# Performance work log

Hardware: AMD Instinct MI355X
Metric: run time of the kernel (lower is better)

Reference implementation:

```python
import jax, jax.numpy as jnp
import numpy as np

B, T, D, H = 512, 128, 128, 256  # batch, time_steps, features, hidden; T == D keeps the source's transpose/step quirk shape-consistent


def _lin_init(k, out_f, in_f):
    s = 1.0 / np.sqrt(in_f)
    k1, k2 = jax.random.split(k)
    w = jax.random.uniform(k1, (out_f, in_f), minval=-s, maxval=s, dtype=jnp.float32)
    b = jax.random.uniform(k2, (out_f,), minval=-s, maxval=s, dtype=jnp.float32)
    return w, b


def setup_inputs() -> dict:
    key = jax.random.key(0)
    ks = jax.random.split(key, 12)
    mask = (jax.random.uniform(ks[0], (B, T, D)) > 0.3).astype(jnp.float32)
    meas = jax.random.normal(ks[1], (B, T, D), dtype=jnp.float32)
    delta = jax.random.uniform(ks[2], (B, T, D), dtype=jnp.float32) * 5.0
    # interleave Mask/Measurement/Delta along dim 1: X[:, 0::3] == mask, etc.
    X = jnp.stack([mask, meas, delta], axis=2).reshape(B, 3 * T, D)
    X_mean = jax.random.normal(ks[3], (1, D, T), dtype=jnp.float32) * 0.1
    din = 2 * T + H  # cat(x, h, mask) per-step input size
    Wz, bz = _lin_init(ks[4], H, din)
    Wr, br = _lin_init(ks[5], H, din)
    Wh, bh = _lin_init(ks[6], H, din)
    Wgx, bgx = _lin_init(ks[7], T, T)   # FilterLinear (identity filter)
    Wgh, bgh = _lin_init(ks[8], H, T)
    Wfc, bfc = _lin_init(ks[9], 1, H)
    gamma_bn = jnp.ones((H,), jnp.float32)
    beta_bn = jnp.zeros((H,), jnp.float32)
    return dict(X=X, X_mean=X_mean, Wz=Wz, bz=bz, Wr=Wr, br=br, Wh=Wh, bh=bh,
                Wgx=Wgx, bgx=bgx, Wgh=Wgh, bgh=bgh,
                gamma_bn=gamma_bn, beta_bn=beta_bn, Wfc=Wfc, bfc=bfc)


def _grud_forward(X, X_mean, Wz, bz, Wr, br, Wh, bh, Wgx, bgx, Wgh, bgh,
                  gamma_bn, beta_bn, Wfc, bfc):
    Bs = X.shape[0]
    Mask = jnp.swapaxes(X[:, 0::3, :], 1, 2)  # (B, D, T) -- source scans over dim 1 after transpose
    Meas = jnp.swapaxes(X[:, 1::3, :], 1, 2)
    Delt = jnp.swapaxes(X[:, 2::3, :], 1, 2)
    # FilterLinear: weight elementwise-masked by identity
    Wgx_eff = jnp.eye(Wgx.shape[0], dtype=Wgx.dtype) * Wgx
    xs = (jnp.moveaxis(Meas, 1, 0),   # (steps, B, T); x_last_obsv == Measurement in the source
          jnp.moveaxis(Mask, 1, 0),
          jnp.moveaxis(Delt, 1, 0),
          X_mean[0])                  # (steps, T)
    h0 = jnp.zeros((Bs, Wgh.shape[0]), dtype=X.dtype)

    def step(h, inp):
        x, m, d, xm = inp
        dx = jnp.exp(-jax.nn.relu(d @ Wgx_eff.T + bgx))   # input decay
        dh = jnp.exp(-jax.nn.relu(d @ Wgh.T + bgh))       # hidden decay
        x = m * x + (1 - m) * (dx * x + (1 - dx) * xm[None, :])  # masked imputation (x_last_obsv == x)
        h = dh * h
        c = jnp.concatenate([x, h, m], axis=1)
        z = jax.nn.sigmoid(c @ Wz.T + bz)
        r = jax.nn.sigmoid(c @ Wr.T + br)
        ht = jnp.tanh(jnp.concatenate([x, r * h, m], axis=1) @ Wh.T + bh)
        h = (1 - z) * h + z * ht
        return h, None

    hT, _ = jax.lax.scan(step, h0, xs)
    # dropout = identity (eval); BatchNorm1d with batch statistics (train-mode math, biased var)
    mu = hT.mean(axis=0)
    var = ((hT - mu) ** 2).mean(axis=0)
    hn = (hT - mu) / jnp.sqrt(var + 1e-5) * gamma_bn + beta_bn
    return hn @ Wfc.T + bfc  # (B, 1)


def reference(X, X_mean, Wz, bz, Wr, br, Wh, bh, Wgx, bgx, Wgh, bgh,
              gamma_bn, beta_bn, Wfc, bfc):
    return _grud_forward(X, X_mean, Wz, bz, Wr, br, Wh, bh, Wgx, bgx,
                         Wgh, bgh, gamma_bn, beta_bn, Wfc, bfc)
```

## Files before the change

kernel.cpp:

```cpp
#include <hip/hip_runtime.h>
#include <stdint.h>


#define NSTEP 128
#define NBAT  512

typedef __attribute__((ext_vector_type(8))) short bf16x8;
typedef __attribute__((ext_vector_type(4))) float f32x4;

__device__ __forceinline__ float bf2f(unsigned short u) {
  union { unsigned int i; float f; } v; v.i = ((unsigned int)u) << 16; return v.f;
}
__device__ __forceinline__ unsigned short f2bf(float f) {
  union { float f; unsigned int i; } v; v.f = f;
  unsigned int x = v.i;
  return (unsigned short)((x + 0x7fffu + ((x >> 16) & 1u)) >> 16);
}
__device__ __forceinline__ unsigned int cvt_pk_bf16(float lo, float hi) {
  unsigned int r;
  asm("v_cvt_pk_bf16_f32 %0, %1, %2" : "=v"(r) : "v"(lo), "v"(hi));
  return r;
}
__device__ __forceinline__ float sigm(float x) { return 1.f / (1.f + __expf(-x)); }
__device__ __forceinline__ unsigned short us4_get(ushort4 v, int r) {
  return r == 0 ? v.x : r == 1 ? v.y : r == 2 ? v.z : v.w;
}
#define PINV(x) asm volatile("" : "+v"(x))
#define BSYNC() do { asm volatile("s_waitcnt lgkmcnt(0)" ::: "memory"); \
                     __builtin_amdgcn_s_barrier(); } while (0)

#define L2E  1.44269504088896f
#define L2E2 2.88539008177793f

__global__ void pack_w(const float* __restrict__ Wz, const float* __restrict__ Wr,
                       const float* __restrict__ Wh, const float* __restrict__ Wgh,
                       const float* __restrict__ bz, const float* __restrict__ br,
                       const float* __restrict__ bh, const float* __restrict__ bgh,
                       const float* __restrict__ Xmean,
                       unsigned short* __restrict__ Wpre, unsigned short* __restrict__ Wzrh,
                       unsigned short* __restrict__ WhhP, float* __restrict__ Bpre,
                       float* __restrict__ XmT) {
  int id = blockIdx.x * 256 + threadIdx.x;
  if (id < 1024 * 384) {
    int j = id / 384, k = id % 384;
    float v = 0.f;
    if (j < 768) {
      const float* W = (j < 256) ? Wz : (j < 512) ? Wr : Wh;
      int jj = j & 255;
      if (k < 128)      v = W[jj * 512 + k];
      else if (k < 256) v = W[jj * 512 + 384 + (k - 128)];
      v *= (j < 512) ? L2E : L2E2;
    } else {
      int jj = j - 768;
      if (k >= 256) v = Wgh[jj * 128 + (k - 256)];
    }
    Wpre[id] = f2bf(v);
    return;
  }
  int id2 = id - 1024 * 384;
  if (id2 < 512 * 256) {
    int j = id2 >> 8, i = id2 & 255;
    float v = (j < 256) ? Wz[j * 512 + 128 + i] : Wr[(j - 256) * 512 + 128 + i];
    Wzrh[id2] = f2bf(v * L2E);
    return;
  }
  int id3 = id2 - 512 * 256;
  if (id3 < 256 * 256) {
    int j = id3 >> 8, i = id3 & 255;
    WhhP[id3] = f2bf(Wh[j * 512 + 128 + i] * L2E2);
    return;
  }
  int id4 = id3 - 256 * 256;
  if (id4 < 1024) {
    float v = (id4 < 256) ? bz[id4] * L2E : (id4 < 512) ? br[id4 - 256] * L2E
            : (id4 < 768) ? bh[id4 - 512] * L2E2 : bgh[id4 - 768];
    Bpre[id4] = v;
    return;
  }
  int id5 = id4 - 1024;
  if (id5 < 128 * 128) {
    int t = id5 >> 7, s = id5 & 127;
    XmT[t * 128 + s] = Xmean[s * 128 + t];
  }
}

__global__ __launch_bounds__(128) void prep(const float* __restrict__ X,
                                            const float* __restrict__ XmT,
                                            const float* __restrict__ Wgx,
                                            const float* __restrict__ bgx,
                                            unsigned short* __restrict__ Cin) {
  __shared__ unsigned short lx[64][132], lm[64][132], ldl[64][132];
  int b = blockIdx.x >> 1, tc = blockIdx.x & 1;
  int s = threadIdx.x;
  const float* Xb = X + (size_t)b * 384 * 128;
  for (int tt = 0; tt < 64; ++tt) {
    int t = tc * 64 + tt;
    float m = Xb[(3 * t + 0) * 128 + s];
    float x = Xb[(3 * t + 1) * 128 + s];
    float d = Xb[(3 * t + 2) * 128 + s];
    float wg = Wgx[t * 128 + t];
    float bg = bgx[t];
    float dx = __expf(-fmaxf(d * wg + bg, 0.f));
    float xm = XmT[t * 128 + s];
    float xt = m * x + (1.f - m) * (dx * x + (1.f - dx) * xm);
    lx[tt][s]  = f2bf(xt);
    lm[tt][s]  = f2bf(m);
    ldl[tt][s] = f2bf(d);
  }
  __syncthreads();
  for (int s0 = 0; s0 < 128; s0 += 2) {
    int ss = s0 + (threadIdx.x >> 6);
    int t  = threadIdx.x & 63;
    size_t base = ((size_t)ss * NBAT + b) * 384;
    Cin[base +       tc * 64 + t] = lx[t][ss];
    Cin[base + 128 + tc * 64 + t] = lm[t][ss];
    Cin[base + 256 + tc * 64 + t] = ldl[t][ss];
  }
}

__global__ __launch_bounds__(256) void u_gemm(const unsigned short* __restrict__ Cin,
                                              const unsigned short* __restrict__ Wpre,
                                              const float* __restrict__ Bpre,
                                              unsigned short* __restrict__ Upre) {
  __shared__ unsigned short Ash[64][392];
  int s  = blockIdx.x >> 3;
  int bc = blockIdx.x & 7;
  int b0 = bc * 64;
  {
    int r = threadIdx.x >> 2, part = threadIdx.x & 3;
    const uint4* src = (const uint4*)(Cin + ((size_t)s * NBAT + b0 + r) * 384);
    uint4* dst = (uint4*)&Ash[r][0];
#pragma unroll
    for (int q = 0; q < 12; ++q) dst[part + q * 4] = src[part + q * 4];
  }
  __syncthreads();
  int wid = threadIdx.x >> 6, lane = threadIdx.x & 63;
  int col = lane & 15, kq = lane >> 4;

  if (wid < 3) {
    int jbase = wid * 256;
    bf16x8 af[4][8];
#pragma unroll
    for (int mt = 0; mt < 4; ++mt)
#pragma unroll
      for (int kt = 0; kt < 8; ++kt)
        af[mt][kt] = *(const bf16x8*)&Ash[mt * 16 + col][kt * 32 + kq * 8];
    for (int jt = 0; jt < 16; ++jt) {
      int j0 = jbase + jt * 16;
      const unsigned short* wrow = Wpre + (size_t)(j0 + col) * 384 + kq * 8;
      f32x4 C[4] = {{0,0,0,0},{0,0,0,0},{0,0,0,0},{0,0,0,0}};
#pragma unroll
      for (int kt = 0; kt < 8; ++kt) {
        bf16x8 bw = *(const bf16x8*)(wrow + kt * 32);
        C[0] = __builtin_amdgcn_mfma_f32_16x16x32_bf16(bw, af[0][kt], C[0], 0, 0, 0);
        C[1] = __builtin_amdgcn_mfma_f32_16x16x32_bf16(bw, af[1][kt], C[1], 0, 0, 0);
        C[2] = __builtin_amdgcn_mfma_f32_16x16x32_bf16(bw, af[2][kt], C[2], 0, 0, 0);
        C[3] = __builtin_amdgcn_mfma_f32_16x16x32_bf16(bw, af[3][kt], C[3], 0, 0, 0);
      }
      int jv = j0 + kq * 4;
      float4 bias = *(const float4*)&Bpre[jv];
#pragma unroll
      for (int mt = 0; mt < 4; ++mt) {
        int bt = bc * 4 + mt;
        ushort4 o;
        o.x = f2bf(C[mt][0] + bias.x); o.y = f2bf(C[mt][1] + bias.y);
        o.z = f2bf(C[mt][2] + bias.z); o.w = f2bf(C[mt][3] + bias.w);
        *(ushort4*)(Upre + (((size_t)s * 32 + bt) * 16 + col) * 1024 + jv) = o;
      }
    }
  } else {
    bf16x8 af[4][4];
#pragma unroll
    for (int mt = 0; mt < 4; ++mt)
#pragma unroll
      for (int kt = 0; kt < 4; ++kt)
        af[mt][kt] = *(const bf16x8*)&Ash[mt * 16 + col][256 + kt * 32 + kq * 8];
    for (int jt = 0; jt < 16; ++jt) {
      int j0 = 768 + jt * 16;
      const unsigned short* wrow = Wpre + (size_t)(j0 + col) * 384 + 256 + kq * 8;
      f32x4 C[4] = {{0,0,0,0},{0,0,0,0},{0,0,0,0},{0,0,0,0}};
#pragma unroll
      for (int kt = 0; kt < 4; ++kt) {
        bf16x8 bw = *(const bf16x8*)(wrow + kt * 32);
        C[0] = __builtin_amdgcn_mfma_f32_16x16x32_bf16(bw, af[0][kt], C[0], 0, 0, 0);
        C[1] = __builtin_amdgcn_mfma_f32_16x16x32_bf16(bw, af[1][kt], C[1], 0, 0, 0);
        C[2] = __builtin_amdgcn_mfma_f32_16x16x32_bf16(bw, af[2][kt], C[2], 0, 0, 0);
        C[3] = __builtin_amdgcn_mfma_f32_16x16x32_bf16(bw, af[3][kt], C[3], 0, 0, 0);
      }
      int jv = j0 + kq * 4;
      float4 bias = *(const float4*)&Bpre[jv];
#pragma unroll
      for (int mt = 0; mt < 4; ++mt) {
        int bt = bc * 4 + mt;
        ushort4 o;
        o.x = f2bf(__expf(-fmaxf(C[mt][0] + bias.x, 0.f)));
        o.y = f2bf(__expf(-fmaxf(C[mt][1] + bias.y, 0.f)));
        o.z = f2bf(__expf(-fmaxf(C[mt][2] + bias.z, 0.f)));
        o.w = f2bf(__expf(-fmaxf(C[mt][3] + bias.w, 0.f)));
        *(ushort4*)(Upre + (((size_t)s * 32 + bt) * 16 + col) * 1024 + jv) = o;
      }
    }
  }
}

__global__ __launch_bounds__(512, 2) void recur(const unsigned short* __restrict__ Upre,
                                                const unsigned short* __restrict__ Wzrh,
                                                const unsigned short* __restrict__ WhhP,
                                                float* __restrict__ hT) {
  __shared__ unsigned short hb[16 * 256];
  __shared__ unsigned short qb[16 * 256];
  __shared__ unsigned short WhL[65536];
  int bt = blockIdx.x, tid = threadIdx.x;
  int wid = tid >> 6, lane = tid & 63, col = lane & 15, kq = lane >> 4;
  const int hsw = (col & 7) << 4;

#pragma unroll
  for (int i = 0; i < 16; ++i) {
    int f = tid + i * 512;
    int row = f >> 5, c = f & 31;
    bf16x8 v = *(const bf16x8*)(WhhP + (size_t)f * 8);
    *(bf16x8*)((char*)WhL + row * 512 + ((c * 16) ^ ((row & 7) << 4))) = v;
  }
  for (int i = tid; i < 16 * 256; i += 512) hb[i] = 0;

  bf16x8 wzf[2][8], wrf[2][8];
#pragma unroll
  for (int mt = 0; mt < 2; ++mt)
#pragma unroll
    for (int kt = 0; kt < 8; ++kt) {
      int j = wid * 32 + mt * 16 + col;
      wzf[mt][kt] = *(const bf16x8*)(Wzrh + (size_t)j * 256 + kt * 32 + kq * 8);
      wrf[mt][kt] = *(const bf16x8*)(Wzrh + (size_t)(256 + j) * 256 + kt * 32 + kq * 8);
      PINV(wzf[mt][kt]);
      PINV(wrf[mt][kt]);
    }

  const int joff0 = wid * 32 + kq * 4;
  const int hs_lo = hsw & 48, hs_hi = hsw & 64;
  const int cq  = (kq * 16) ^ hs_lo;
  const int rbA = col * 512 + cq + hs_hi;
  const int rbB = col * 512 + cq - hs_hi;
  const int row0 = wid * 32 + col;
  const int wrbA = row0 * 512 + cq + hs_hi;
  const int wrbB = row0 * 512 + cq - hs_hi;
  const int wby0 = col * 512 + ((joff0 * 2) ^ hsw);
  const int wby1 = col * 512 + (((joff0 + 16) * 2) ^ hsw);

  const unsigned short* Ub0 = Upre + ((size_t)bt * 16 + col) * 1024;
  const size_t SS = 32 * 16 * 1024;

  ushort4 uz[2], ur[2], uh[2], ug[2];
#pragma unroll
  for (int mt = 0; mt < 2; ++mt) {
    uz[mt] = *(const ushort4*)(Ub0 + 0   + joff0 + mt * 16);
    ur[mt] = *(const ushort4*)(Ub0 + 256 + joff0 + mt * 16);
    uh[mt] = *(const ushort4*)(Ub0 + 512 + joff0 + mt * 16);
    ug[mt] = *(const ushort4*)(Ub0 + SS + 768 + joff0 + mt * 16);
  }
  const unsigned short* pnext = Ub0 + SS + joff0;
  const unsigned short* pg    = Ub0 + 2 * SS + 768 + joff0;
  f32x4 Hst[2] = {{0,0,0,0},{0,0,0,0}};
  float zk[2][4];
  BSYNC();

  for (int s = 0; s < NSTEP; ++s) {
    f32x4 Cz[2] = {{0,0,0,0},{0,0,0,0}}, Cr[2] = {{0,0,0,0},{0,0,0,0}};
#pragma unroll
    for (int kt = 0; kt < 8; ++kt) {
      bf16x8 b = *(const bf16x8*)((const char*)hb + ((kt & 1) ? rbB : rbA) + kt * 64);
      Cz[0] = __builtin_amdgcn_mfma_f32_16x16x32_bf16(wzf[0][kt], b, Cz[0], 0, 0, 0);
      Cr[0] = __builtin_amdgcn_mfma_f32_16x16x32_bf16(wrf[0][kt], b, Cr[0], 0, 0, 0);
      Cz[1] = __builtin_amdgcn_mfma_f32_16x16x32_bf16(wzf[1][kt], b, Cz[1], 0, 0, 0);
      Cr[1] = __builtin_amdgcn_mfma_f32_16x16x32_bf16(wrf[1][kt], b, Cr[1], 0, 0, 0);
    }
#pragma unroll
    for (int mt = 0; mt < 2; ++mt) {
      float qv[4];
#pragma unroll
      for (int r = 0; r < 4; ++r) {
        float xz = Cz[mt][r] + bf2f(us4_get(uz[mt], r));
        float xr = Cr[mt][r] + bf2f(us4_get(ur[mt], r));
        float zv = __builtin_amdgcn_rcpf(1.f + __builtin_amdgcn_exp2f(-xz));
        float rv = __builtin_amdgcn_rcpf(1.f + __builtin_amdgcn_exp2f(-xr));
        zk[mt][r] = zv;
        qv[r] = rv * Hst[mt][r];
      }
      uint2 qw;
      qw.x = cvt_pk_bf16(qv[0], qv[1]);
      qw.y = cvt_pk_bf16(qv[2], qv[3]);
      *(uint2*)((char*)qb + (mt ? wby1 : wby0)) = qw;
    }
#pragma unroll
    for (int mt = 0; mt < 2; ++mt) {
      uz[mt] = *(const ushort4*)(pnext + 0   + mt * 16);
      ur[mt] = *(const ushort4*)(pnext + 256 + mt * 16);
    }
    BSYNC();
    f32x4 Ch[2] = {{0,0,0,0},{0,0,0,0}};
#pragma unroll
    for (int kt = 0; kt < 8; ++kt) {
      int ro = ((kt & 1) ? rbB : rbA) + kt * 64;
      int wo = ((kt & 1) ? wrbB : wrbA) + kt * 64;
      bf16x8 b  = *(const bf16x8*)((const char*)qb + ro);
      bf16x8 w0 = *(const bf16x8*)((const char*)WhL + wo);
      bf16x8 w1 = *(const bf16x8*)((const char*)WhL + wo + 16 * 512);
      Ch[0] = __builtin_amdgcn_mfma_f32_16x16x32_bf16(w0, b, Ch[0], 0, 0, 0);
      Ch[1] = __builtin_amdgcn_mfma_f32_16x16x32_bf16(w1, b, Ch[1], 0, 0, 0);
    }
#pragma unroll
    for (int mt = 0; mt < 2; ++mt) {
      float hn[4];
#pragma unroll
      for (int r = 0; r < 4; ++r) {
        float p = Ch[mt][r] + bf2f(us4_get(uh[mt], r));
        float e = __builtin_amdgcn_exp2f(p);
        float rr = __builtin_amdgcn_rcpf(e + 1.f);
        float th = fmaf(-2.f, rr, 1.f);
        float H = Hst[mt][r];
        hn[r] = fmaf(zk[mt][r], th - H, H);
      }
      if (s < NSTEP - 1) {
        float Hn[4];
#pragma unroll
        for (int r = 0; r < 4; ++r) {
          Hn[r] = hn[r] * bf2f(us4_get(ug[mt], r));
          Hst[mt][r] = Hn[r];
        }
        uint2 hw;
        hw.x = cvt_pk_bf16(Hn[0], Hn[1]);
        hw.y = cvt_pk_bf16(Hn[2], Hn[3]);
        *(uint2*)((char*)hb + (mt ? wby1 : wby0)) = hw;
      } else {
        float4 o4; o4.x = hn[0]; o4.y = hn[1]; o4.z = hn[2]; o4.w = hn[3];
        *(float4*)&hT[((size_t)bt * 16 + col) * 256 + joff0 + mt * 16] = o4;
      }
    }
#pragma unroll
    for (int mt = 0; mt < 2; ++mt) {
      uh[mt] = *(const ushort4*)(pnext + 512 + mt * 16);
      ug[mt] = *(const ushort4*)(pg + mt * 16);
    }
    pnext += SS;
    pg += SS;
    BSYNC();
  }
}

__global__ __launch_bounds__(64) void bn_stats(const float* __restrict__ hT,
                                               const float* __restrict__ gamma,
                                               const float* __restrict__ beta,
                                               const float* __restrict__ Wfc,
                                               const float* __restrict__ bfc,
                                               float* __restrict__ av) {
  int j = blockIdx.x, lane = threadIdx.x;
  float sum = 0.f, sum2 = 0.f;
#pragma unroll
  for (int b = lane; b < NBAT; b += 64) {
    float v = hT[(size_t)b * 256 + j];
    sum += v; sum2 += v * v;
  }
  for (int o = 32; o; o >>= 1) {
    sum  += __shfl_down(sum, o);
    sum2 += __shfl_down(sum2, o);
  }
  if (lane == 0) {
    float mu = sum * (1.f / NBAT);
    float var = sum2 * (1.f / NBAT) - mu * mu;
    float a = gamma[j] * Wfc[j] * rsqrtf(var + 1e-5f);
    av[j] = a;
    float c = beta[j] * Wfc[j] - a * mu + (j == 0 ? bfc[0] : 0.f);
    atomicAdd(&av[256], c);
  }
}

__global__ __launch_bounds__(64) void fin(const float* __restrict__ hT,
                                          const float* __restrict__ av,
                                          float* __restrict__ out) {
  int b = blockIdx.x, lane = threadIdx.x;
  float4 hv = *(const float4*)&hT[(size_t)b * 256 + lane * 4];
  float4 a  = *(const float4*)&av[lane * 4];
  float d = hv.x * a.x + hv.y * a.y + hv.z * a.z + hv.w * a.w;
  for (int o = 32; o; o >>= 1) d += __shfl_down(d, o);
  if (lane == 0) out[b] = d + av[256];
}

extern "C" void kernel_launch(void* const* d_in, const int* in_sizes, int n_in,
                              void* d_out, int out_size, void* d_ws, size_t ws_size,
                              hipStream_t stream) {
  (void)in_sizes; (void)n_in; (void)out_size; (void)ws_size;
  const float* X     = (const float*)d_in[0];
  const float* Xmean = (const float*)d_in[1];
  const float* Wz    = (const float*)d_in[2];
  const float* bz    = (const float*)d_in[3];
  const float* Wr    = (const float*)d_in[4];
  const float* br    = (const float*)d_in[5];
  const float* Wh    = (const float*)d_in[6];
  const float* bh    = (const float*)d_in[7];
  const float* Wgx   = (const float*)d_in[8];
  const float* bgx   = (const float*)d_in[9];
  const float* Wgh   = (const float*)d_in[10];
  const float* bgh   = (const float*)d_in[11];
  const float* gamma = (const float*)d_in[12];
  const float* beta  = (const float*)d_in[13];
  const float* Wfc   = (const float*)d_in[14];
  const float* bfc   = (const float*)d_in[15];
  float* out = (float*)d_out;
  char* ws = (char*)d_ws;

  unsigned short* Upre = (unsigned short*)(ws + 0ull);
  unsigned short* Cin  = (unsigned short*)(ws + 134217728ull);
  unsigned short* Wpre = (unsigned short*)(ws + 184549376ull);
  unsigned short* Wzrh = (unsigned short*)(ws + 185335808ull);
  unsigned short* WhhP = (unsigned short*)(ws + 185597952ull);
  float*          Bpre = (float*)(ws + 185729024ull);
  float*          hT   = (float*)(ws + 185733120ull);
  float*          av   = (float*)(ws + 186257408ull);
  float*          XmT  = (float*)(ws + 186259456ull);

  pack_w<<<2372, 256, 0, stream>>>(Wz, Wr, Wh, Wgh, bz, br, bh, bgh, Xmean,
                                   Wpre, Wzrh, WhhP, Bpre, XmT);
  prep<<<1024, 128, 0, stream>>>(X, XmT, Wgx, bgx, Cin);
  u_gemm<<<1024, 256, 0, stream>>>(Cin, Wpre, Bpre, Upre);
  recur<<<32, 512, 0, stream>>>(Upre, Wzrh, WhhP, hT);
  hipMemsetAsync((char*)av + 256 * sizeof(float), 0, sizeof(float), stream);
  bn_stats<<<256, 64, 0, stream>>>(hT, gamma, beta, Wfc, bfc, av);
  fin<<<512, 64, 0, stream>>>(hT, av, out);
}
```

Before: 424.1 us.

## Split recurrence across 16 waves per block, one 16-column tile each

The recurrent kernel now launches 1024 threads per block instead of 512, so each wave owns one 16-wide hidden tile instead of two. This halves the per-wave MFMA chain and elementwise work per step, shortening the serial critical path of each time step. Pinned z/r weight fragments move to AGPRs via an 'a' constraint to relieve VGPR pressure at the higher wave count. The cost is more waves meeting at each barrier, which adds sync overhead, and LDS traffic for the shared Wh weights grows with the extra waves.

```diff
diff --git a/kernel.cpp b/kernel.cpp
--- a/kernel.cpp
+++ b/kernel.cpp
@@ -21,11 +21,10 @@
   asm("v_cvt_pk_bf16_f32 %0, %1, %2" : "=v"(r) : "v"(lo), "v"(hi));
   return r;
 }
-__device__ __forceinline__ float sigm(float x) { return 1.f / (1.f + __expf(-x)); }
 __device__ __forceinline__ unsigned short us4_get(ushort4 v, int r) {
   return r == 0 ? v.x : r == 1 ? v.y : r == 2 ? v.z : v.w;
 }
-#define PINV(x) asm volatile("" : "+v"(x))
+#define PINA(x) asm volatile("" : "+a"(x))
 #define BSYNC() do { asm volatile("s_waitcnt lgkmcnt(0)" ::: "memory"); \
                      __builtin_amdgcn_s_barrier(); } while (0)
 
@@ -203,10 +202,10 @@
   }
 }
 
-__global__ __launch_bounds__(512, 2) void recur(const unsigned short* __restrict__ Upre,
-                                                const unsigned short* __restrict__ Wzrh,
-                                                const unsigned short* __restrict__ WhhP,
-                                                float* __restrict__ hT) {
+__global__ __launch_bounds__(1024, 4) void recur(const unsigned short* __restrict__ Upre,
+                                                 const unsigned short* __restrict__ Wzrh,
+                                                 const unsigned short* __restrict__ WhhP,
+                                                 float* __restrict__ hT) {
   __shared__ unsigned short hb[16 * 256];
   __shared__ unsigned short qb[16 * 256];
   __shared__ unsigned short WhL[65536];
@@ -215,131 +214,113 @@
   const int hsw = (col & 7) << 4;
 
 #pragma unroll
-  for (int i = 0; i < 16; ++i) {
-    int f = tid + i * 512;
+  for (int i = 0; i < 8; ++i) {
+    int f = tid + i * 1024;
     int row = f >> 5, c = f & 31;
     bf16x8 v = *(const bf16x8*)(WhhP + (size_t)f * 8);
     *(bf16x8*)((char*)WhL + row * 512 + ((c * 16) ^ ((row & 7) << 4))) = v;
   }
-  for (int i = tid; i < 16 * 256; i += 512) hb[i] = 0;
-
-  bf16x8 wzf[2][8], wrf[2][8];
-#pragma unroll
-  for (int mt = 0; mt < 2; ++mt)
-#pragma unroll
-    for (int kt = 0; kt < 8; ++kt) {
-      int j = wid * 32 + mt * 16 + col;
-      wzf[mt][kt] = *(const bf16x8*)(Wzrh + (size_t)j * 256 + kt * 32 + kq * 8);
-      wrf[mt][kt] = *(const bf16x8*)(Wzrh + (size_t)(256 + j) * 256 + kt * 32 + kq * 8);
-      PINV(wzf[mt][kt]);
-      PINV(wrf[mt][kt]);
-    }
-
-  const int joff0 = wid * 32 + kq * 4;
+  for (int i = tid; i < 16 * 256; i += 1024) hb[i] = 0;
+
+  bf16x8 wzf[8], wrf[8];
+#pragma unroll
+  for (int kt = 0; kt < 8; ++kt) {
+    int j = wid * 16 + col;
+    wzf[kt] = *(const bf16x8*)(Wzrh + (size_t)j * 256 + kt * 32 + kq * 8);
+    wrf[kt] = *(const bf16x8*)(Wzrh + (size_t)(256 + j) * 256 + kt * 32 + kq * 8);
+    PINA(wzf[kt]);
+    PINA(wrf[kt]);
+  }
+
+  const int joff0 = wid * 16 + kq * 4;
   const int hs_lo = hsw & 48, hs_hi = hsw & 64;
   const int cq  = (kq * 16) ^ hs_lo;
   const int rbA = col * 512 + cq + hs_hi;
   const int rbB = col * 512 + cq - hs_hi;
-  const int row0 = wid * 32 + col;
+  const int row0 = wid * 16 + col;
   const int wrbA = row0 * 512 + cq + hs_hi;
   const int wrbB = row0 * 512 + cq - hs_hi;
-  const int wby0 = col * 512 + ((joff0 * 2) ^ hsw);
-  const int wby1 = col * 512 + (((joff0 + 16) * 2) ^ hsw);
+  const int wby = col * 512 + ((joff0 * 2) ^ hsw);
 
   const unsigned short* Ub0 = Upre + ((size_t)bt * 16 + col) * 1024;
   const size_t SS = 32 * 16 * 1024;
 
-  ushort4 uz[2], ur[2], uh[2], ug[2];
-#pragma unroll
-  for (int mt = 0; mt < 2; ++mt) {
-    uz[mt] = *(const ushort4*)(Ub0 + 0   + joff0 + mt * 16);
-    ur[mt] = *(const ushort4*)(Ub0 + 256 + joff0 + mt * 16);
-    uh[mt] = *(const ushort4*)(Ub0 + 512 + joff0 + mt * 16);
-    ug[mt] = *(const ushort4*)(Ub0 + SS + 768 + joff0 + mt * 16);
-  }
+  ushort4 uz, ur, uh, ug;
+  uz = *(const ushort4*)(Ub0 + 0   + joff0);
+  ur = *(const ushort4*)(Ub0 + 256 + joff0);
+  uh = *(const ushort4*)(Ub0 + 512 + joff0);
+  ug = *(const ushort4*)(Ub0 + SS + 768 + joff0);
   const unsigned short* pnext = Ub0 + SS + joff0;
   const unsigned short* pg    = Ub0 + 2 * SS + 768 + joff0;
-  f32x4 Hst[2] = {{0,0,0,0},{0,0,0,0}};
-  float zk[2][4];
+  f32x4 Hst = {0, 0, 0, 0};
+  float zk[4];
   BSYNC();
 
   for (int s = 0; s < NSTEP; ++s) {
-    f32x4 Cz[2] = {{0,0,0,0},{0,0,0,0}}, Cr[2] = {{0,0,0,0},{0,0,0,0}};
+    f32x4 Cz = {0,0,0,0}, Cr = {0,0,0,0};
 #pragma unroll
     for (int kt = 0; kt < 8; ++kt) {
       bf16x8 b = *(const bf16x8*)((const char*)hb + ((kt & 1) ? rbB : rbA) + kt * 64);
-      Cz[0] = __builtin_amdgcn_mfma_f32_16x16x32_bf16(wzf[0][kt], b, Cz[0], 0, 0, 0);
-      Cr[0] = __builtin_amdgcn_mfma_f32_16x16x32_bf16(wrf[0][kt], b, Cr[0], 0, 0, 0);
-      Cz[1] = __builtin_amdgcn_mfma_f32_16x16x32_bf16(wzf[1][kt], b, Cz[1], 0, 0, 0);
-      Cr[1] = __builtin_amdgcn_mfma_f32_16x16x32_bf16(wrf[1][kt], b, Cr[1], 0, 0, 0);
-    }
-#pragma unroll
-    for (int mt = 0; mt < 2; ++mt) {
+      Cz = __builtin_amdgcn_mfma_f32_16x16x32_bf16(wzf[kt], b, Cz, 0, 0, 0);
+      Cr = __builtin_amdgcn_mfma_f32_16x16x32_bf16(wrf[kt], b, Cr, 0, 0, 0);
+    }
+    {
       float qv[4];
 #pragma unroll
       for (int r = 0; r < 4; ++r) {
-        float xz = Cz[mt][r] + bf2f(us4_get(uz[mt], r));
-        float xr = Cr[mt][r] + bf2f(us4_get(ur[mt], r));
+        float xz = Cz[r] + bf2f(us4_get(uz, r));
+        float xr = Cr[r] + bf2f(us4_get(ur, r));
         float zv = __builtin_amdgcn_rcpf(1.f + __builtin_amdgcn_exp2f(-xz));
         float rv = __builtin_amdgcn_rcpf(1.f + __builtin_amdgcn_exp2f(-xr));
-        zk[mt][r] = zv;
-        qv[r] = rv * Hst[mt][r];
+        zk[r] = zv;
+        qv[r] = rv * Hst[r];
       }
       uint2 qw;
       qw.x = cvt_pk_bf16(qv[0], qv[1]);
       qw.y = cvt_pk_bf16(qv[2], qv[3]);
-      *(uint2*)((char*)qb + (mt ? wby1 : wby0)) = qw;
-    }
-#pragma unroll
-    for (int mt = 0; mt < 2; ++mt) {
-      uz[mt] = *(const ushort4*)(pnext + 0   + mt * 16);
-      ur[mt] = *(const ushort4*)(pnext + 256 + mt * 16);
-    }
+      *(uint2*)((char*)qb + wby) = qw;
+    }
+    uz = *(const ushort4*)(pnext + 0);
+    ur = *(const ushort4*)(pnext + 256);
     BSYNC();
-    f32x4 Ch[2] = {{0,0,0,0},{0,0,0,0}};
+    f32x4 Ch = {0,0,0,0};
 #pragma unroll
     for (int kt = 0; kt < 8; ++kt) {
       int ro = ((kt & 1) ? rbB : rbA) + kt * 64;
       int wo = ((kt & 1) ? wrbB : wrbA) + kt * 64;
-      bf16x8 b  = *(const bf16x8*)((const char*)qb + ro);
-      bf16x8 w0 = *(const bf16x8*)((const char*)WhL + wo);
-      bf16x8 w1 = *(const bf16x8*)((const char*)WhL + wo + 16 * 512);
-      Ch[0] = __builtin_amdgcn_mfma_f32_16x16x32_bf16(w0, b, Ch[0], 0, 0, 0);
-      Ch[1] = __builtin_amdgcn_mfma_f32_16x16x32_bf16(w1, b, Ch[1], 0, 0, 0);
-    }
-#pragma unroll
-    for (int mt = 0; mt < 2; ++mt) {
+      bf16x8 b = *(const bf16x8*)((const char*)qb + ro);
+      bf16x8 w = *(const bf16x8*)((const char*)WhL + wo);
+      Ch = __builtin_amdgcn_mfma_f32_16x16x32_bf16(w, b, Ch, 0, 0, 0);
+    }
+    {
       float hn[4];
 #pragma unroll
       for (int r = 0; r < 4; ++r) {
-        float p = Ch[mt][r] + bf2f(us4_get(uh[mt], r));
+        float p = Ch[r] + bf2f(us4_get(uh, r));
         float e = __builtin_amdgcn_exp2f(p);
         float rr = __builtin_amdgcn_rcpf(e + 1.f);
         float th = fmaf(-2.f, rr, 1.f);
-        float H = Hst[mt][r];
-        hn[r] = fmaf(zk[mt][r], th - H, H);
+        float H = Hst[r];
+        hn[r] = fmaf(zk[r], th - H, H);
       }
       if (s < NSTEP - 1) {
         float Hn[4];
 #pragma unroll
         for (int r = 0; r < 4; ++r) {
-          Hn[r] = hn[r] * bf2f(us4_get(ug[mt], r));
-          Hst[mt][r] = Hn[r];
+          Hn[r] = hn[r] * bf2f(us4_get(ug, r));
+          Hst[r] = Hn[r];
         }
         uint2 hw;
         hw.x = cvt_pk_bf16(Hn[0], Hn[1]);
         hw.y = cvt_pk_bf16(Hn[2], Hn[3]);
-        *(uint2*)((char*)hb + (mt ? wby1 : wby0)) = hw;
+        *(uint2*)((char*)hb + wby) = hw;
       } else {
         float4 o4; o4.x = hn[0]; o4.y = hn[1]; o4.z = hn[2]; o4.w = hn[3];
-        *(float4*)&hT[((size_t)bt * 16 + col) * 256 + joff0 + mt * 16] = o4;
-      }
-    }
-#pragma unroll
-    for (int mt = 0; mt < 2; ++mt) {
-      uh[mt] = *(const ushort4*)(pnext + 512 + mt * 16);
-      ug[mt] = *(const ushort4*)(pg + mt * 16);
-    }
+        *(float4*)&hT[((size_t)bt * 16 + col) * 256 + joff0] = o4;
+      }
+    }
+    uh = *(const ushort4*)(pnext + 512);
+    ug = *(const ushort4*)(pg);
     pnext += SS;
     pg += SS;
     BSYNC();
@@ -421,7 +402,7 @@
                                    Wpre, Wzrh, WhhP, Bpre, XmT);
   prep<<<1024, 128, 0, stream>>>(X, XmT, Wgx, bgx, Cin);
   u_gemm<<<1024, 256, 0, stream>>>(Cin, Wpre, Bpre, Upre);
-  recur<<<32, 512, 0, stream>>>(Upre, Wzrh, WhhP, hT);
+  recur<<<32, 1024, 0, stream>>>(Upre, Wzrh, WhhP, hT);
   hipMemsetAsync((char*)av + 256 * sizeof(float), 0, sizeof(float), stream);
   bn_stats<<<256, 64, 0, stream>>>(hT, gamma, beta, Wfc, bfc, av);
   fin<<<512, 64, 0, stream>>>(hT, av, out);
```

Result: no change. 426.4 us (+0.6%).
